# Performance work log

Measured on AMD Instinct MI355X. Metric: run time of the kernel, lower is better.

The kernel has to match this reference:

```python
import jax, jax.numpy as jnp
import numpy as np

H = 16          # num attention heads (== num kv heads here)
D = 128         # head_dim
HID = 2048      # hidden_size = H * D
THETA = 10000.0
SCALE = 1.0 / (D ** 0.5)
EPS = 1e-8


def rotate_half(x):
    x1, x2 = x[..., : D // 2], x[..., D // 2 :]
    return jnp.concatenate((-x2, x1), axis=-1)


def rope_tables(seq_len):
    inv_freq = 1.0 / (THETA ** (jnp.arange(0, D, 2, dtype=jnp.float32) / D))
    freqs = jnp.outer(jnp.arange(seq_len, dtype=jnp.float32), inv_freq)  # [S, D/2]
    emb = jnp.concatenate((freqs, freqs), axis=-1)                        # [S, D]
    return jnp.cos(emb), jnp.sin(emb)


def setup_inputs() -> dict:
    key = jax.random.key(0)
    ks = jax.random.split(key, 10)
    B, S = 1, 2048
    hidden_states = jax.random.normal(ks[0], (B, S, HID), jnp.float32) * 0.02
    position_ids = jnp.tile(jnp.arange(S, dtype=jnp.int32)[None, :], (B, 1))
    # additive causal mask, shape (B, 1, S, S) as asserted in the torch forward
    causal = jnp.tril(jnp.ones((S, S), dtype=bool))
    attention_mask = jnp.where(causal, 0.0, -1e9).astype(jnp.float32)[None, None]
    attention_mask = jnp.tile(attention_mask, (B, 1, 1, 1))
    Wq = jax.random.normal(ks[1], (HID, HID), jnp.float32) * 0.02
    bq = jax.random.normal(ks[2], (HID,), jnp.float32) * 0.02
    Wk = jax.random.normal(ks[3], (HID, HID), jnp.float32) * 0.02
    bk = jax.random.normal(ks[4], (HID,), jnp.float32) * 0.02
    Wo = jax.random.normal(ks[5], (HID, HID), jnp.float32) * 0.02
    beta = jax.random.normal(ks[6], (1,), jnp.float32)
    M = jax.random.normal(ks[7], (H, D, D), jnp.float32) * 0.02
    z = jax.random.uniform(ks[8], (H, D), jnp.float32) * 100.0 + 1.0  # positive accumulator
    return {
        "hidden_states": hidden_states,
        "attention_mask": attention_mask,
        "position_ids": position_ids,
        "Wq": Wq, "bq": bq, "Wk": Wk, "bk": bk, "Wo": Wo,
        "beta": beta, "M": M, "z": z,
    }


def reference(hidden_states, attention_mask, position_ids, Wq, bq, Wk, bk, Wo, beta, M, z):
    B, S, _ = hidden_states.shape
    # projections (NOTE: source uses q_proj for value_states too -- reproduced faithfully)
    q = (hidden_states @ Wq + bq).reshape(B, S, H, D).transpose(0, 2, 1, 3)  # [B,H,S,D]
    k = (hidden_states @ Wk + bk).reshape(B, S, H, D).transpose(0, 2, 1, 3)
    v = q  # value_states = q_proj(hidden_states), no RoPE applied to values

    cos, sin = rope_tables(S)
    cos = cos[position_ids][:, None]  # [B,1,S,D]
    sin = sin[position_ids][:, None]
    qr = q * cos + rotate_half(q) * sin
    kr = k * cos + rotate_half(k) * sin

    # --- compressive memory retrieval (with pre-update M, z) ---
    sq = jax.nn.elu(qr) + 1.0                                  # [B,H,S,D]
    mem_num = jnp.einsum('bhsd,hde->bhse', sq, M)              # [B,H,S,D]
    mem_den = jnp.einsum('bhsd,hd->bhs', sq, z)[..., None] + EPS
    memory_output = mem_num / mem_den

    # --- memory update: outer-product accumulation ---
    sk = jax.nn.elu(kr) + 1.0
    M_new = M + jnp.einsum('bhsd,bhse->hde', sk, v)
    z_new = z + sk.sum(axis=(0, 2))

    # --- local attention (SDPA with additive mask, dropout 0) ---
    scores = jnp.einsum('bhsd,bhtd->bhst', qr, kr) * SCALE + attention_mask
    probs = jax.nn.softmax(scores, axis=-1)
    attn_output = jnp.einsum('bhst,bhtd->bhsd', probs, v)

    # --- long-term memory injection: sigmoid-gated blend ---
    g = jax.nn.sigmoid(beta)[0]
    combined = g * memory_output + (1.0 - g) * attn_output     # [B,H,S,D]
    combined = combined.transpose(0, 2, 1, 3).reshape(B, S, HID)
    final_output = combined @ Wo
    return (final_output, M_new, z_new)
```

## Files before the change

### kernel.cpp

```cpp
#include <hip/hip_runtime.h>
#include <hip/hip_bf16.h>


#define S_LEN 2048
#define HID 2048
#define NH 16
#define HD 128
#define SCALE_QK 0.088388347648318447f

typedef __attribute__((ext_vector_type(8))) short bf16x8;
typedef __attribute__((ext_vector_type(4))) float f32x4;

__device__ __forceinline__ short f2bf(float f) {
  __hip_bfloat16 h = __float2bfloat16(f);
  return __builtin_bit_cast(short, h);
}
__device__ __forceinline__ float bf2f(short s) {
  unsigned int u = ((unsigned int)(unsigned short)s) << 16;
  return __builtin_bit_cast(float, u);
}
__device__ __forceinline__ void gload16(const void* g, void* l) {
  __builtin_amdgcn_global_load_lds(
      (const __attribute__((address_space(1))) void*)g,
      (__attribute__((address_space(3))) void*)l, 16, 0, 0);
}

__global__ __launch_bounds__(256) void f32_to_bf16_kernel(
    const float* __restrict__ in, short* __restrict__ out) {
  size_t i = (size_t)(blockIdx.x * 256 + threadIdx.x) * 8;
  float4 a = *reinterpret_cast<const float4*>(in + i);
  float4 b = *reinterpret_cast<const float4*>(in + i + 4);
  alignas(16) short t[8] = {f2bf(a.x), f2bf(a.y), f2bf(a.z), f2bf(a.w),
                            f2bf(b.x), f2bf(b.y), f2bf(b.z), f2bf(b.w)};
  *reinterpret_cast<int4*>(out + i) = *reinterpret_cast<int4*>(t);
}

__global__ __launch_bounds__(256) void transpose_f2b_kernel(
    const float* __restrict__ in, short* __restrict__ out, int R, int C) {
  __shared__ float t[32][33];
  size_t bo = (size_t)blockIdx.z * R * C;
  int r0 = blockIdx.y * 32, c0 = blockIdx.x * 32;
  int tx = threadIdx.x & 31, ty = threadIdx.x >> 5;
#pragma unroll
  for (int i = 0; i < 4; ++i)
    t[ty + i * 8][tx] = in[bo + (size_t)(r0 + ty + i * 8) * C + c0 + tx];
  __syncthreads();
#pragma unroll
  for (int i = 0; i < 4; ++i)
    out[bo + (size_t)(c0 + ty + i * 8) * R + r0 + tx] = f2bf(t[tx][ty + i * 8]);
}

__global__ __launch_bounds__(256) void transpose_b2b_kernel(
    const short* __restrict__ in, short* __restrict__ out, int R, int C) {
  __shared__ short t[32][33];
  int r0 = blockIdx.y * 32, c0 = blockIdx.x * 32;
  int tx = threadIdx.x & 31, ty = threadIdx.x >> 5;
#pragma unroll
  for (int i = 0; i < 4; ++i)
    t[ty + i * 8][tx] = in[(size_t)(r0 + ty + i * 8) * C + c0 + tx];
  __syncthreads();
#pragma unroll
  for (int i = 0; i < 4; ++i)
    out[(size_t)(c0 + ty + i * 8) * R + r0 + tx] = t[tx][ty + i * 8];
}

__global__ __launch_bounds__(256) void tables_kernel(
    const int* __restrict__ pos_ids, float* __restrict__ cost,
    float* __restrict__ sint) {
  int idx = blockIdx.x * 256 + threadIdx.x;
  int s = idx >> 6, j = idx & 63;
  float pos = (float)pos_ids[s];
  float inv = powf(10000.0f, -((float)j) / 64.0f);
  float a = pos * inv;
  cost[idx] = cosf(a);
  sint[idx] = sinf(a);
}

__global__ __launch_bounds__(256) void gemm_qk_rope_kernel(
    const short* __restrict__ A, const short* __restrict__ BT,
    const float* __restrict__ bq, const float* __restrict__ bk,
    const float* __restrict__ cost, const float* __restrict__ sint,
    short* __restrict__ qr, short* __restrict__ kr, short* __restrict__ sq,
    short* __restrict__ sk, short* __restrict__ v) {
  __shared__ __align__(16) char smem[67584];
  const int K = 2048;
  const int tid = threadIdx.x;
  const int wave = tid >> 6, lane = tid & 63;
  const int g = lane >> 4, l15 = lane & 15;
  const int wm = (wave >> 1) * 64, wn = (wave & 1) * 64;
  const int row0 = blockIdx.x * 128;
  const int colg0 = blockIdx.y * 128;

  const int ld_r = wave * 32 + (lane >> 3);
  const int ld_c = (lane & 7) * 8;
  const short* Ag = A + (size_t)(row0 + ld_r) * K + ld_c;
  const short* Bg = BT + (size_t)(colg0 + ld_r) * K + ld_c;

#define GSTAGE(BUF, KT)                                                       \
  {                                                                           \
    _Pragma("unroll") for (int i = 0; i < 4; ++i) {                           \
      gload16(Ag + (size_t)(KT) * 64 + (size_t)i * 8 * 2048,                  \
              smem + (BUF) * 32768 + wave * 4096 + i * 1024);                 \
      gload16(Bg + (size_t)(KT) * 64 + (size_t)i * 8 * 2048,                  \
              smem + (BUF) * 32768 + 16384 + wave * 4096 + i * 1024);         \
    }                                                                         \
  }

  f32x4 acc[4][4] = {};
  GSTAGE(0, 0);
  __syncthreads();
  for (int kt = 0; kt < 32; ++kt) {
    const int cur = kt & 1;
    if (kt + 1 < 32) GSTAGE(cur ^ 1, kt + 1);
#pragma unroll
    for (int ks = 0; ks < 2; ++ks) {
      bf16x8 a[4], b[4];
#pragma unroll
      for (int m = 0; m < 4; ++m)
        a[m] = *reinterpret_cast<bf16x8*>(smem + cur * 32768 +
                                          (wm + m * 16 + l15) * 128 +
                                          (ks * 32 + g * 8) * 2);
#pragma unroll
      for (int n = 0; n < 4; ++n)
        b[n] = *reinterpret_cast<bf16x8*>(smem + cur * 32768 + 16384 +
                                          (wn + n * 16 + l15) * 128 +
                                          (ks * 32 + g * 8) * 2);
#pragma unroll
      for (int m = 0; m < 4; ++m)
#pragma unroll
        for (int n = 0; n < 4; ++n)
          acc[m][n] = __builtin_amdgcn_mfma_f32_16x16x32_bf16(a[m], b[n],
                                                              acc[m][n], 0, 0, 0);
    }
    __syncthreads();
  }
#undef GSTAGE

  const bool qpath = (colg0 < 2048);
  const int col0 = qpath ? colg0 : colg0 - 2048;
  const float* bias = qpath ? bq : bk;
  float* qb = reinterpret_cast<float*>(smem);
#pragma unroll
  for (int m = 0; m < 4; ++m)
#pragma unroll
    for (int n = 0; n < 4; ++n) {
      int rl = wm + m * 16 + g * 4;
      int cl = wn + n * 16 + l15;
      float bv = bias[col0 + cl];
#pragma unroll
      for (int r = 0; r < 4; ++r) qb[(rl + r) * 132 + cl] = acc[m][n][r] + bv;
    }
  __syncthreads();

  const int rl = tid >> 1;
  const int c0 = (tid & 1) * 64;
  const int rowg = row0 + rl;
  const float sgn = (c0 == 0) ? -1.0f : 1.0f;
  const size_t obase = (size_t)rowg * HID + col0 + c0;
#pragma unroll
  for (int j0 = 0; j0 < 64; j0 += 8) {
    alignas(16) short o1[8], o2[8], o3[8];
#pragma unroll
    for (int jj = 0; jj < 8; ++jj) {
      int j = j0 + jj;
      float self = qb[rl * 132 + c0 + j];
      float part = qb[rl * 132 + (c0 ^ 64) + j];
      float cs = cost[rowg * 64 + j];
      float sn = sint[rowg * 64 + j];
      float rv = self * cs + sgn * part * sn;
      o1[jj] = f2bf(rv);
      o2[jj] = f2bf(rv > 0.0f ? rv + 1.0f : __expf(rv));
      o3[jj] = f2bf(self);
    }
    if (qpath) {
      *reinterpret_cast<int4*>(qr + obase + j0) = *reinterpret_cast<int4*>(o1);
      *reinterpret_cast<int4*>(sq + obase + j0) = *reinterpret_cast<int4*>(o2);
      *reinterpret_cast<int4*>(v + obase + j0) = *reinterpret_cast<int4*>(o3);
    } else {
      *reinterpret_cast<int4*>(kr + obase + j0) = *reinterpret_cast<int4*>(o1);
      *reinterpret_cast<int4*>(sk + obase + j0) = *reinterpret_cast<int4*>(o2);
    }
  }
}

__global__ __launch_bounds__(256) void gemm_wo_kernel(
    const short* __restrict__ A, const short* __restrict__ BT,
    float* __restrict__ C) {
  __shared__ __align__(16) char smem[65536];
  const int K = 2048;
  const int tid = threadIdx.x;
  const int wave = tid >> 6, lane = tid & 63;
  const int g = lane >> 4, l15 = lane & 15;
  const int wm = (wave >> 1) * 64, wn = (wave & 1) * 64;
  const int row0 = blockIdx.x * 128;
  const int col0 = blockIdx.y * 128;

  const int ld_r = wave * 32 + (lane >> 3);
  const int ld_c = (lane & 7) * 8;
  const short* Ag = A + (size_t)(row0 + ld_r) * K + ld_c;
  const short* Bg = BT + (size_t)(col0 + ld_r) * K + ld_c;

#define GSTAGE(BUF, KT)                                                       \
  {                                                                           \
    _Pragma("unroll") for (int i = 0; i < 4; ++i) {                           \
      gload16(Ag + (size_t)(KT) * 64 + (size_t)i * 8 * 2048,                  \
              smem + (BUF) * 32768 + wave * 4096 + i * 1024);                 \
      gload16(Bg + (size_t)(KT) * 64 + (size_t)i * 8 * 2048,                  \
              smem + (BUF) * 32768 + 16384 + wave * 4096 + i * 1024);         \
    }                                                                         \
  }

  f32x4 acc[4][4] = {};
  GSTAGE(0, 0);
  __syncthreads();
  for (int kt = 0; kt < 32; ++kt) {
    const int cur = kt & 1;
    if (kt + 1 < 32) GSTAGE(cur ^ 1, kt + 1);
#pragma unroll
    for (int ks = 0; ks < 2; ++ks) {
      bf16x8 a[4], b[4];
#pragma unroll
      for (int m = 0; m < 4; ++m)
        a[m] = *reinterpret_cast<bf16x8*>(smem + cur * 32768 +
                                          (wm + m * 16 + l15) * 128 +
                                          (ks * 32 + g * 8) * 2);
#pragma unroll
      for (int n = 0; n < 4; ++n)
        b[n] = *reinterpret_cast<bf16x8*>(smem + cur * 32768 + 16384 +
                                          (wn + n * 16 + l15) * 128 +
                                          (ks * 32 + g * 8) * 2);
#pragma unroll
      for (int m = 0; m < 4; ++m)
#pragma unroll
        for (int n = 0; n < 4; ++n)
          acc[m][n] = __builtin_amdgcn_mfma_f32_16x16x32_bf16(a[m], b[n],
                                                              acc[m][n], 0, 0, 0);
    }
    __syncthreads();
  }
#undef GSTAGE

#pragma unroll
  for (int m = 0; m < 4; ++m)
#pragma unroll
    for (int n = 0; n < 4; ++n) {
      int row = row0 + wm + m * 16 + g * 4;
      int col = col0 + wn + n * 16 + l15;
#pragma unroll
      for (int r = 0; r < 4; ++r)
        C[(size_t)(row + r) * 2048 + col] = acc[m][n][r];
    }
}

__global__ __launch_bounds__(256) void attn_kernel(
    const short* __restrict__ qr, const short* __restrict__ kr,
    const short* __restrict__ vT, const short* __restrict__ sq,
    const short* __restrict__ MT, const float* __restrict__ z,
    const float* __restrict__ beta, short* __restrict__ comb) {
  __shared__ short k_s[2][64 * 128];
  __shared__ short v_s[2][128 * 64];
  __shared__ short p_s[4][16 * 64];
  const int tid = threadIdx.x;
  const int wave = tid >> 6, lane = tid & 63;
  const int g = lane >> 4, l15 = lane & 15;
  const int bid = blockIdx.x;
  const int h = bid & 15;
  const int u = bid >> 4;
  const int qt = (u < 16) ? (2 * u) : (31 - 2 * (u - 16));
  const int q0 = qt * 64;
  const int ntiles = qt + 1;

  const int krow_b = wave * 16 + (lane >> 4);
  const int vrow_b = wave * 32 + (lane >> 3);
#define STAGE_TILE(B, T0)                                                     \
  {                                                                           \
    _Pragma("unroll") for (int i = 0; i < 4; ++i) {                           \
      int rk = krow_b + i * 4;                                                \
      int ck = (lane & 15) ^ (rk & 7);                                        \
      gload16(kr + (size_t)((T0) + rk) * HID + h * HD + ck * 8,               \
              &k_s[B][0] + wave * 2048 + i * 512);                            \
      int rv = vrow_b + i * 8;                                                \
      int cv = (lane & 7) ^ (rv & 7);                                         \
      gload16(vT + (size_t)(h * HD + rv) * S_LEN + (T0) + cv * 8,             \
              &v_s[B][0] + wave * 2048 + i * 512);                            \
    }                                                                         \
  }

  bf16x8 qf[4];
#pragma unroll
  for (int ks = 0; ks < 4; ++ks) {
    int row = q0 + wave * 16 + l15;
    qf[ks] = *reinterpret_cast<const bf16x8*>(qr + (size_t)row * HID + h * HD +
                                              ks * 32 + g * 8);
  }

  STAGE_TILE(0, 0);
  __syncthreads();

  f32x4 o[8] = {};
  float m_run[4], l_run[4];
#pragma unroll
  for (int r = 0; r < 4; ++r) {
    m_run[r] = -3.0e38f;
    l_run[r] = 0.0f;
  }

  for (int kt = 0; kt < ntiles; ++kt) {
    const int cur = kt & 1;
    if (kt + 1 < ntiles) STAGE_TILE(cur ^ 1, (kt + 1) * 64);

    f32x4 sfr[4] = {};
    __builtin_amdgcn_s_setprio(1);
#pragma unroll
    for (int n = 0; n < 4; ++n) {
#pragma unroll
      for (int ks = 0; ks < 4; ++ks) {
        int rr = n * 16 + l15;
        int off = (rr * 256 + (ks * 32 + g * 8) * 2) ^ ((rr & 7) << 4);
        bf16x8 b =
            *reinterpret_cast<bf16x8*>(reinterpret_cast<char*>(k_s[cur]) + off);
        sfr[n] = __builtin_amdgcn_mfma_f32_16x16x32_bf16(qf[ks], b, sfr[n], 0,
                                                         0, 0);
      }
    }
    __builtin_amdgcn_s_setprio(0);

    const bool diag = (kt == qt);
#pragma unroll
    for (int r = 0; r < 4; ++r) {
      const int srow = q0 + wave * 16 + g * 4 + r;
      float mx = m_run[r];
#pragma unroll
      for (int n = 0; n < 4; ++n) {
        float val = sfr[n][r] * SCALE_QK;
        if (diag) {
          int t = kt * 64 + n * 16 + l15;
          val = (t <= srow) ? val : -3.0e38f;
        }
        sfr[n][r] = val;
        mx = fmaxf(mx, val);
      }
      mx = fmaxf(mx, __shfl_xor(mx, 1));
      mx = fmaxf(mx, __shfl_xor(mx, 2));
      mx = fmaxf(mx, __shfl_xor(mx, 4));
      mx = fmaxf(mx, __shfl_xor(mx, 8));
      float sum = 0.0f;
#pragma unroll
      for (int n = 0; n < 4; ++n) {
        float p = __expf(sfr[n][r] - mx);
        sfr[n][r] = p;
        sum += p;
      }
      sum += __shfl_xor(sum, 1);
      sum += __shfl_xor(sum, 2);
      sum += __shfl_xor(sum, 4);
      sum += __shfl_xor(sum, 8);
      float f = __expf(m_run[r] - mx);
      l_run[r] = l_run[r] * f + sum;
      m_run[r] = mx;
#pragma unroll
      for (int n = 0; n < 8; ++n) o[n][r] *= f;
    }

    char* pw = reinterpret_cast<char*>(p_s[wave]);
#pragma unroll
    for (int n = 0; n < 4; ++n)
#pragma unroll
      for (int r = 0; r < 4; ++r) {
        int rl = g * 4 + r;
        int off = (rl * 128 + (n * 16 + l15) * 2) ^ ((rl & 7) << 4);
        *reinterpret_cast<short*>(pw + off) = f2bf(sfr[n][r]);
      }

    __builtin_amdgcn_s_setprio(1);
#pragma unroll
    for (int ks = 0; ks < 2; ++ks) {
      int offp = (l15 * 128 + (ks * 32 + g * 8) * 2) ^ ((l15 & 7) << 4);
      bf16x8 pa = *reinterpret_cast<bf16x8*>(pw + offp);
#pragma unroll
      for (int n = 0; n < 8; ++n) {
        int rr = n * 16 + l15;
        int off = (rr * 128 + (ks * 32 + g * 8) * 2) ^ ((rr & 7) << 4);
        bf16x8 vb =
            *reinterpret_cast<bf16x8*>(reinterpret_cast<char*>(v_s[cur]) + off);
        o[n] = __builtin_amdgcn_mfma_f32_16x16x32_bf16(pa, vb, o[n], 0, 0, 0);
      }
    }
    __builtin_amdgcn_s_setprio(0);

    __syncthreads();
  }
#undef STAGE_TILE

  short* mt_s = &k_s[0][0];
#pragma unroll
  for (int i = 0; i < 8; ++i) {
    int c = tid + 256 * i;
    int r = c >> 4, kc = c & 15;
    int4 d = *reinterpret_cast<const int4*>(MT + (size_t)h * 16384 + r * 128 +
                                            kc * 8);
    *reinterpret_cast<int4*>(reinterpret_cast<char*>(mt_s) +
                             ((r * 256 + kc * 16) ^ ((r & 7) << 4))) = d;
  }
  __syncthreads();

  bf16x8 af[4];
#pragma unroll
  for (int ks = 0; ks < 4; ++ks) {
    int row = q0 + wave * 16 + l15;
    af[ks] = *reinterpret_cast<const bf16x8*>(sq + (size_t)row * HID + h * HD +
                                              ks * 32 + g * 8);
  }
  f32x4 acc2[8] = {};
#pragma unroll
  for (int ks = 0; ks < 4; ++ks) {
#pragma unroll
    for (int n = 0; n < 8; ++n) {
      int rr = n * 16 + l15;
      int off = (rr * 256 + (ks * 32 + g * 8) * 2) ^ ((rr & 7) << 4);
      bf16x8 b =
          *reinterpret_cast<bf16x8*>(reinterpret_cast<char*>(mt_s) + off);
      acc2[n] = __builtin_amdgcn_mfma_f32_16x16x32_bf16(af[ks], b, acc2[n], 0,
                                                        0, 0);
    }
  }

  float den[4];
#pragma unroll
  for (int r = 0; r < 4; ++r) {
    int row = q0 + wave * 16 + g * 4 + r;
    bf16x8 sv = *reinterpret_cast<const bf16x8*>(sq + (size_t)row * HID +
                                                 h * HD + l15 * 8);
    float part = 0.0f;
#pragma unroll
    for (int j = 0; j < 8; ++j) part += bf2f(sv[j]) * z[h * HD + l15 * 8 + j];
    part += __shfl_xor(part, 1);
    part += __shfl_xor(part, 2);
    part += __shfl_xor(part, 4);
    part += __shfl_xor(part, 8);
    den[r] = part + 1e-8f;
  }

  float gv = 1.0f / (1.0f + __expf(-beta[0]));
#pragma unroll
  for (int n = 0; n < 8; ++n)
#pragma unroll
    for (int r = 0; r < 4; ++r) {
      int row = q0 + wave * 16 + g * 4 + r;
      int col = n * 16 + l15;
      float mem = acc2[n][r] / den[r];
      float at = o[n][r] / l_run[r];
      comb[(size_t)row * HID + h * HD + col] = f2bf(gv * mem + (1.0f - gv) * at);
    }
}

__global__ __launch_bounds__(256) void mnew_part_kernel(
    const short* __restrict__ skT, const short* __restrict__ vT,
    float* __restrict__ part) {
  const int sp = blockIdx.x;
  const int h = blockIdx.y;
  const int tid = threadIdx.x;
  const int wave = tid >> 6, lane = tid & 63;
  const int g = lane >> 4, l15 = lane & 15;
  f32x4 acc[2][8] = {};
  for (int ks = sp * 8; ks < sp * 8 + 8; ++ks) {
    bf16x8 a[2];
#pragma unroll
    for (int m = 0; m < 2; ++m) {
      int dd = wave * 32 + m * 16 + l15;
      a[m] = *reinterpret_cast<const bf16x8*>(skT + (size_t)(h * HD + dd) * S_LEN +
                                              ks * 32 + g * 8);
    }
#pragma unroll
    for (int n = 0; n < 8; ++n) {
      int e = n * 16 + l15;
      bf16x8 b = *reinterpret_cast<const bf16x8*>(
          vT + (size_t)(h * HD + e) * S_LEN + ks * 32 + g * 8);
#pragma unroll
      for (int m = 0; m < 2; ++m)
        acc[m][n] =
            __builtin_amdgcn_mfma_f32_16x16x32_bf16(a[m], b, acc[m][n], 0, 0, 0);
    }
  }
#pragma unroll
  for (int m = 0; m < 2; ++m)
#pragma unroll
    for (int n = 0; n < 8; ++n)
#pragma unroll
      for (int r = 0; r < 4; ++r) {
        int dd = wave * 32 + m * 16 + g * 4 + r;
        int e = n * 16 + l15;
        part[(size_t)(sp * 16 + h) * 16384 + (size_t)dd * 128 + e] =
            acc[m][n][r];
      }
}

__global__ __launch_bounds__(256) void mnew_reduce_kernel(
    const float* __restrict__ part, const float* __restrict__ Mold,
    float* __restrict__ Mout) {
  int idx = blockIdx.x * 256 + threadIdx.x;
  int j4 = idx * 4;
  int h = j4 >> 14;
  int rem = j4 & 16383;
  float4 a = *reinterpret_cast<const float4*>(Mold + j4);
#pragma unroll
  for (int s = 0; s < 8; ++s) {
    float4 p = *reinterpret_cast<const float4*>(
        part + ((size_t)(s * 16 + h) << 14) + rem);
    a.x += p.x;
    a.y += p.y;
    a.z += p.z;
    a.w += p.w;
  }
  *reinterpret_cast<float4*>(Mout + j4) = a;
}

__global__ __launch_bounds__(256) void znew_kernel(const short* __restrict__ skT,
                                                   const float* __restrict__ z,
                                                   float* __restrict__ out) {
  int row = blockIdx.x;
  int tid = threadIdx.x;
  bf16x8 vv = *reinterpret_cast<const bf16x8*>(skT + (size_t)row * S_LEN + tid * 8);
  float s = 0.0f;
#pragma unroll
  for (int j = 0; j < 8; ++j) s += bf2f(vv[j]);
#pragma unroll
  for (int off = 1; off < 64; off <<= 1) s += __shfl_xor(s, off);
  __shared__ float wsum[4];
  if ((tid & 63) == 0) wsum[tid >> 6] = s;
  __syncthreads();
  if (tid == 0) out[row] = z[row] + wsum[0] + wsum[1] + wsum[2] + wsum[3];
}

extern "C" void kernel_launch(void* const* d_in, const int* in_sizes, int n_in,
                              void* d_out, int out_size, void* d_ws,
                              size_t ws_size, hipStream_t stream) {
  const float* hs = (const float*)d_in[0];
  const int* pos = (const int*)d_in[2];
  const float* Wq = (const float*)d_in[3];
  const float* bq = (const float*)d_in[4];
  const float* Wk = (const float*)d_in[5];
  const float* bk = (const float*)d_in[6];
  const float* Wo = (const float*)d_in[7];
  const float* beta = (const float*)d_in[8];
  const float* Mm = (const float*)d_in[9];
  const float* z = (const float*)d_in[10];
  float* out = (float*)d_out;

  char* ws = (char*)d_ws;
  const size_t MB = 1u << 20;
  short* hs_b = (short*)(ws + 0);
  short* WqkT = (short*)(ws + 8 * MB);
  short* WoT = (short*)(ws + 24 * MB);
  short* qr = (short*)(ws + 32 * MB);
  short* kr = (short*)(ws + 40 * MB);
  short* sq = (short*)(ws + 48 * MB);
  short* sk = (short*)(ws + 56 * MB);
  short* v = (short*)(ws + 64 * MB);
  short* comb = (short*)(ws + 72 * MB);
  short* MT = (short*)(ws + 80 * MB);
  float* cost = (float*)(ws + 80 * MB + 512 * 1024);
  float* sint = (float*)(ws + 81 * MB);
  short* skT = WqkT;
  short* vT = WqkT + 4 * 1024 * 1024;
  float* mpart = (float*)hs_b;

  f32_to_bf16_kernel<<<2048, 256, 0, stream>>>(hs, hs_b);
  transpose_f2b_kernel<<<dim3(64, 64, 1), 256, 0, stream>>>(Wq, WqkT, 2048, 2048);
  transpose_f2b_kernel<<<dim3(64, 64, 1), 256, 0, stream>>>(
      Wk, WqkT + 4 * 1024 * 1024, 2048, 2048);
  transpose_f2b_kernel<<<dim3(64, 64, 1), 256, 0, stream>>>(Wo, WoT, 2048, 2048);
  transpose_f2b_kernel<<<dim3(4, 4, 16), 256, 0, stream>>>(Mm, MT, 128, 128);
  tables_kernel<<<512, 256, 0, stream>>>(pos, cost, sint);

  gemm_qk_rope_kernel<<<dim3(16, 32), 256, 0, stream>>>(
      hs_b, WqkT, bq, bk, cost, sint, qr, kr, sq, sk, v);
  transpose_b2b_kernel<<<dim3(64, 64, 1), 256, 0, stream>>>(v, vT, 2048, 2048);
  transpose_b2b_kernel<<<dim3(64, 64, 1), 256, 0, stream>>>(sk, skT, 2048, 2048);

  attn_kernel<<<512, 256, 0, stream>>>(qr, kr, vT, sq, MT, z, beta, comb);
  gemm_wo_kernel<<<dim3(16, 16), 256, 0, stream>>>(comb, WoT, out);
  mnew_part_kernel<<<dim3(8, 16), 256, 0, stream>>>(skT, vT, mpart);
  mnew_reduce_kernel<<<256, 256, 0, stream>>>(mpart, Mm, out + 4194304);
  znew_kernel<<<2048, 256, 0, stream>>>(skT, z, out + 4194304 + 16 * 128 * 128);
}
```

Before: 356.8 us.

## Split causal attention KV range across blocks, fuse transposes into QK epilogue

The QK projection epilogue now writes skT and vT directly in transposed layout, which removes the two standalone bf16 transpose kernels. Attention now uses 512-thread blocks covering 128 query rows, with the KV range split into two halves that run as separate blocks. Each half writes partial outputs plus its running max and sum, and a new combine kernel merges them and applies the memory retrieval and gating. This is meant to balance causal work across blocks and cut transpose traffic, at the cost of extra partial-output round trips through memory and one more launch. Online softmax also skips rescaling unless the running max grows by more than 8.

New measurement: 368.8 us. +3.4%, slower.

```diff
diff --git a/kernel.cpp b/kernel.cpp
--- a/kernel.cpp
+++ b/kernel.cpp
@@ -48,20 +48,6 @@
 #pragma unroll
   for (int i = 0; i < 4; ++i)
     out[bo + (size_t)(c0 + ty + i * 8) * R + r0 + tx] = f2bf(t[tx][ty + i * 8]);
-}
-
-__global__ __launch_bounds__(256) void transpose_b2b_kernel(
-    const short* __restrict__ in, short* __restrict__ out, int R, int C) {
-  __shared__ short t[32][33];
-  int r0 = blockIdx.y * 32, c0 = blockIdx.x * 32;
-  int tx = threadIdx.x & 31, ty = threadIdx.x >> 5;
-#pragma unroll
-  for (int i = 0; i < 4; ++i)
-    t[ty + i * 8][tx] = in[(size_t)(r0 + ty + i * 8) * C + c0 + tx];
-  __syncthreads();
-#pragma unroll
-  for (int i = 0; i < 4; ++i)
-    out[(size_t)(c0 + ty + i * 8) * R + r0 + tx] = t[tx][ty + i * 8];
 }
 
 __global__ __launch_bounds__(256) void tables_kernel(
@@ -81,9 +67,8 @@
     const float* __restrict__ bq, const float* __restrict__ bk,
     const float* __restrict__ cost, const float* __restrict__ sint,
     short* __restrict__ qr, short* __restrict__ kr, short* __restrict__ sq,
-    short* __restrict__ sk, short* __restrict__ v) {
+    short* __restrict__ skT, short* __restrict__ vT) {
   __shared__ __align__(16) char smem[67584];
-  const int K = 2048;
   const int tid = threadIdx.x;
   const int wave = tid >> 6, lane = tid & 63;
   const int g = lane >> 4, l15 = lane & 15;
@@ -93,8 +78,8 @@
 
   const int ld_r = wave * 32 + (lane >> 3);
   const int ld_c = (lane & 7) * 8;
-  const short* Ag = A + (size_t)(row0 + ld_r) * K + ld_c;
-  const short* Bg = BT + (size_t)(colg0 + ld_r) * K + ld_c;
+  const short* Ag = A + (size_t)(row0 + ld_r) * 2048 + ld_c;
+  const short* Bg = BT + (size_t)(colg0 + ld_r) * 2048 + ld_c;
 
 #define GSTAGE(BUF, KT)                                                       \
   {                                                                           \
@@ -138,6 +123,7 @@
 
   const bool qpath = (colg0 < 2048);
   const int col0 = qpath ? colg0 : colg0 - 2048;
+  const int hh = col0 >> 7;
   const float* bias = qpath ? bq : bk;
   float* qb = reinterpret_cast<float*>(smem);
 #pragma unroll
@@ -152,33 +138,61 @@
     }
   __syncthreads();
 
-  const int rl = tid >> 1;
-  const int c0 = (tid & 1) * 64;
-  const int rowg = row0 + rl;
-  const float sgn = (c0 == 0) ? -1.0f : 1.0f;
-  const size_t obase = (size_t)rowg * HID + col0 + c0;
-#pragma unroll
-  for (int j0 = 0; j0 < 64; j0 += 8) {
-    alignas(16) short o1[8], o2[8], o3[8];
-#pragma unroll
-    for (int jj = 0; jj < 8; ++jj) {
-      int j = j0 + jj;
-      float self = qb[rl * 132 + c0 + j];
-      float part = qb[rl * 132 + (c0 ^ 64) + j];
-      float cs = cost[rowg * 64 + j];
-      float sn = sint[rowg * 64 + j];
-      float rv = self * cs + sgn * part * sn;
-      o1[jj] = f2bf(rv);
-      o2[jj] = f2bf(rv > 0.0f ? rv + 1.0f : __expf(rv));
-      o3[jj] = f2bf(self);
-    }
-    if (qpath) {
-      *reinterpret_cast<int4*>(qr + obase + j0) = *reinterpret_cast<int4*>(o1);
-      *reinterpret_cast<int4*>(sq + obase + j0) = *reinterpret_cast<int4*>(o2);
-      *reinterpret_cast<int4*>(v + obase + j0) = *reinterpret_cast<int4*>(o3);
-    } else {
-      *reinterpret_cast<int4*>(kr + obase + j0) = *reinterpret_cast<int4*>(o1);
-      *reinterpret_cast<int4*>(sk + obase + j0) = *reinterpret_cast<int4*>(o2);
+  {
+    const int rl = tid >> 1;
+    const int c0 = (tid & 1) * 64;
+    const int rowg = row0 + rl;
+    const float sgn = (c0 == 0) ? -1.0f : 1.0f;
+    const size_t obase = (size_t)rowg * HID + col0 + c0;
+#pragma unroll
+    for (int j0 = 0; j0 < 64; j0 += 8) {
+      alignas(16) short o1[8], o2[8];
+#pragma unroll
+      for (int jj = 0; jj < 8; ++jj) {
+        int j = j0 + jj;
+        float self = qb[rl * 132 + c0 + j];
+        float part = qb[rl * 132 + (c0 ^ 64) + j];
+        float cs = cost[rowg * 64 + j];
+        float sn = sint[rowg * 64 + j];
+        float rv = self * cs + sgn * part * sn;
+        o1[jj] = f2bf(rv);
+        o2[jj] = f2bf(rv > 0.0f ? rv + 1.0f : __expf(rv));
+      }
+      if (qpath) {
+        *reinterpret_cast<int4*>(qr + obase + j0) = *reinterpret_cast<int4*>(o1);
+        *reinterpret_cast<int4*>(sq + obase + j0) = *reinterpret_cast<int4*>(o2);
+      } else {
+        *reinterpret_cast<int4*>(kr + obase + j0) = *reinterpret_cast<int4*>(o1);
+      }
+    }
+  }
+
+  {
+    const int d = tid & 127;
+    const int sc = tid >> 7;
+    const int dp = d ^ 64;
+    const float sgn2 = (d < 64) ? -1.0f : 1.0f;
+    short* dstb = (qpath ? vT : skT) + (size_t)(hh * HD + d) * S_LEN + row0 +
+                  sc * 64;
+#pragma unroll
+    for (int j0 = 0; j0 < 64; j0 += 8) {
+      alignas(16) short ot[8];
+#pragma unroll
+      for (int jj = 0; jj < 8; ++jj) {
+        int s = sc * 64 + j0 + jj;
+        float self = qb[s * 132 + d];
+        if (qpath) {
+          ot[jj] = f2bf(self);
+        } else {
+          float part = qb[s * 132 + dp];
+          int rowg = row0 + s;
+          float cs = cost[rowg * 64 + (d & 63)];
+          float sn = sint[rowg * 64 + (d & 63)];
+          float rv = self * cs + sgn2 * part * sn;
+          ot[jj] = f2bf(rv > 0.0f ? rv + 1.0f : __expf(rv));
+        }
+      }
+      *reinterpret_cast<int4*>(dstb + j0) = *reinterpret_cast<int4*>(ot);
     }
   }
 }
@@ -187,7 +201,6 @@
     const short* __restrict__ A, const short* __restrict__ BT,
     float* __restrict__ C) {
   __shared__ __align__(16) char smem[65536];
-  const int K = 2048;
   const int tid = threadIdx.x;
   const int wave = tid >> 6, lane = tid & 63;
   const int g = lane >> 4, l15 = lane & 15;
@@ -197,8 +210,8 @@
 
   const int ld_r = wave * 32 + (lane >> 3);
   const int ld_c = (lane & 7) * 8;
-  const short* Ag = A + (size_t)(row0 + ld_r) * K + ld_c;
-  const short* Bg = BT + (size_t)(col0 + ld_r) * K + ld_c;
+  const short* Ag = A + (size_t)(row0 + ld_r) * 2048 + ld_c;
+  const short* Bg = BT + (size_t)(col0 + ld_r) * 2048 + ld_c;
 
 #define GSTAGE(BUF, KT)                                                       \
   {                                                                           \
@@ -252,37 +265,38 @@
     }
 }
 
-__global__ __launch_bounds__(256) void attn_kernel(
+__global__ __launch_bounds__(512, 4) void attn_kernel(
     const short* __restrict__ qr, const short* __restrict__ kr,
-    const short* __restrict__ vT, const short* __restrict__ sq,
-    const short* __restrict__ MT, const float* __restrict__ z,
-    const float* __restrict__ beta, short* __restrict__ comb) {
+    const short* __restrict__ vT, short* __restrict__ opart,
+    float* __restrict__ ml) {
   __shared__ short k_s[2][64 * 128];
   __shared__ short v_s[2][128 * 64];
-  __shared__ short p_s[4][16 * 64];
+  __shared__ short p_s[8][16 * 64];
   const int tid = threadIdx.x;
   const int wave = tid >> 6, lane = tid & 63;
   const int g = lane >> 4, l15 = lane & 15;
   const int bid = blockIdx.x;
   const int h = bid & 15;
-  const int u = bid >> 4;
-  const int qt = (u < 16) ? (2 * u) : (31 - 2 * (u - 16));
-  const int q0 = qt * 64;
-  const int ntiles = qt + 1;
-
-  const int krow_b = wave * 16 + (lane >> 4);
-  const int vrow_b = wave * 32 + (lane >> 3);
+  const int w = bid >> 4;
+  const int half = (w < 16) ? 0 : 1;
+  const int qt = (w < 16) ? w : 31 - w;
+  const int q0 = qt * 128;
+  const int jstart = half ? (qt + 1) : 0;
+  const int jend = half ? (2 * qt + 2) : (qt + 1);
+
+  const int krow_b = wave * 8 + (lane >> 4);
+  const int vrow_b = wave * 16 + (lane >> 3);
 #define STAGE_TILE(B, T0)                                                     \
   {                                                                           \
-    _Pragma("unroll") for (int i = 0; i < 4; ++i) {                           \
+    _Pragma("unroll") for (int i = 0; i < 2; ++i) {                           \
       int rk = krow_b + i * 4;                                                \
       int ck = (lane & 15) ^ (rk & 7);                                        \
       gload16(kr + (size_t)((T0) + rk) * HID + h * HD + ck * 8,               \
-              &k_s[B][0] + wave * 2048 + i * 512);                            \
+              &k_s[B][0] + wave * 1024 + i * 512);                            \
       int rv = vrow_b + i * 8;                                                \
       int cv = (lane & 7) ^ (rv & 7);                                         \
       gload16(vT + (size_t)(h * HD + rv) * S_LEN + (T0) + cv * 8,             \
-              &v_s[B][0] + wave * 2048 + i * 512);                            \
+              &v_s[B][0] + wave * 1024 + i * 512);                            \
     }                                                                         \
   }
 
@@ -294,7 +308,7 @@
                                               ks * 32 + g * 8);
   }
 
-  STAGE_TILE(0, 0);
+  STAGE_TILE(0, jstart * 64);
   __syncthreads();
 
   f32x4 o[8] = {};
@@ -305,9 +319,9 @@
     l_run[r] = 0.0f;
   }
 
-  for (int kt = 0; kt < ntiles; ++kt) {
-    const int cur = kt & 1;
-    if (kt + 1 < ntiles) STAGE_TILE(cur ^ 1, (kt + 1) * 64);
+  for (int j = jstart; j < jend; ++j) {
+    const int cur = (j - jstart) & 1;
+    if (j + 1 < jend) STAGE_TILE(cur ^ 1, (j + 1) * 64);
 
     f32x4 sfr[4] = {};
     __builtin_amdgcn_s_setprio(1);
@@ -325,29 +339,36 @@
     }
     __builtin_amdgcn_s_setprio(0);
 
-    const bool diag = (kt == qt);
+    const bool diag = (j >= 2 * qt);
 #pragma unroll
     for (int r = 0; r < 4; ++r) {
       const int srow = q0 + wave * 16 + g * 4 + r;
-      float mx = m_run[r];
+      float pmax = -3.0e38f;
 #pragma unroll
       for (int n = 0; n < 4; ++n) {
         float val = sfr[n][r] * SCALE_QK;
         if (diag) {
-          int t = kt * 64 + n * 16 + l15;
+          int t = j * 64 + n * 16 + l15;
           val = (t <= srow) ? val : -3.0e38f;
         }
         sfr[n][r] = val;
-        mx = fmaxf(mx, val);
-      }
-      mx = fmaxf(mx, __shfl_xor(mx, 1));
-      mx = fmaxf(mx, __shfl_xor(mx, 2));
-      mx = fmaxf(mx, __shfl_xor(mx, 4));
-      mx = fmaxf(mx, __shfl_xor(mx, 8));
+        pmax = fmaxf(pmax, val);
+      }
+      pmax = fmaxf(pmax, __shfl_xor(pmax, 1));
+      pmax = fmaxf(pmax, __shfl_xor(pmax, 2));
+      pmax = fmaxf(pmax, __shfl_xor(pmax, 4));
+      pmax = fmaxf(pmax, __shfl_xor(pmax, 8));
+      if (pmax > m_run[r] + 8.0f) {
+        float f = __expf(m_run[r] - pmax);
+        l_run[r] *= f;
+#pragma unroll
+        for (int n = 0; n < 8; ++n) o[n][r] *= f;
+        m_run[r] = pmax;
+      }
       float sum = 0.0f;
 #pragma unroll
       for (int n = 0; n < 4; ++n) {
-        float p = __expf(sfr[n][r] - mx);
+        float p = __expf(sfr[n][r] - m_run[r]);
         sfr[n][r] = p;
         sum += p;
       }
@@ -355,11 +376,7 @@
       sum += __shfl_xor(sum, 2);
       sum += __shfl_xor(sum, 4);
       sum += __shfl_xor(sum, 8);
-      float f = __expf(m_run[r] - mx);
-      l_run[r] = l_run[r] * f + sum;
-      m_run[r] = mx;
-#pragma unroll
-      for (int n = 0; n < 8; ++n) o[n][r] *= f;
+      l_run[r] += sum;
     }
 
     char* pw = reinterpret_cast<char*>(p_s[wave]);
@@ -392,7 +409,34 @@
   }
 #undef STAGE_TILE
 
-  short* mt_s = &k_s[0][0];
+  const size_t ob = (size_t)half * 4194304;
+#pragma unroll
+  for (int r = 0; r < 4; ++r) {
+    int row = q0 + wave * 16 + g * 4 + r;
+#pragma unroll
+    for (int n = 0; n < 8; ++n) {
+      int col = n * 16 + l15;
+      opart[ob + (size_t)row * HID + h * HD + col] = f2bf(o[n][r]);
+    }
+    if (l15 == 0) {
+      size_t mli = ((size_t)(half * 16 + h) * 2048 + row) * 2;
+      ml[mli] = m_run[r];
+      ml[mli + 1] = l_run[r];
+    }
+  }
+}
+
+__global__ __launch_bounds__(256) void combine_kernel(
+    const short* __restrict__ opart, const float* __restrict__ ml,
+    const short* __restrict__ sq, const short* __restrict__ MT,
+    const float* __restrict__ z, const float* __restrict__ beta,
+    short* __restrict__ comb) {
+  __shared__ short mt_s[128 * 128];
+  const int tid = threadIdx.x;
+  const int wave = tid >> 6, lane = tid & 63;
+  const int g = lane >> 4, l15 = lane & 15;
+  const int h = blockIdx.y;
+  const int s0 = blockIdx.x * 128;
 #pragma unroll
   for (int i = 0; i < 8; ++i) {
     int c = tid + 256 * i;
@@ -404,53 +448,68 @@
   }
   __syncthreads();
 
-  bf16x8 af[4];
+  f32x4 acc[2][8] = {};
 #pragma unroll
   for (int ks = 0; ks < 4; ++ks) {
-    int row = q0 + wave * 16 + l15;
-    af[ks] = *reinterpret_cast<const bf16x8*>(sq + (size_t)row * HID + h * HD +
+    bf16x8 a[2];
+#pragma unroll
+    for (int m = 0; m < 2; ++m) {
+      int row = s0 + wave * 32 + m * 16 + l15;
+      a[m] = *reinterpret_cast<const bf16x8*>(sq + (size_t)row * HID + h * HD +
                                               ks * 32 + g * 8);
-  }
-  f32x4 acc2[8] = {};
-#pragma unroll
-  for (int ks = 0; ks < 4; ++ks) {
+    }
 #pragma unroll
     for (int n = 0; n < 8; ++n) {
       int rr = n * 16 + l15;
       int off = (rr * 256 + (ks * 32 + g * 8) * 2) ^ ((rr & 7) << 4);
-      bf16x8 b =
-          *reinterpret_cast<bf16x8*>(reinterpret_cast<char*>(mt_s) + off);
-      acc2[n] = __builtin_amdgcn_mfma_f32_16x16x32_bf16(af[ks], b, acc2[n], 0,
-                                                        0, 0);
-    }
-  }
-
-  float den[4];
-#pragma unroll
-  for (int r = 0; r < 4; ++r) {
-    int row = q0 + wave * 16 + g * 4 + r;
-    bf16x8 sv = *reinterpret_cast<const bf16x8*>(sq + (size_t)row * HID +
-                                                 h * HD + l15 * 8);
-    float part = 0.0f;
-#pragma unroll
-    for (int j = 0; j < 8; ++j) part += bf2f(sv[j]) * z[h * HD + l15 * 8 + j];
-    part += __shfl_xor(part, 1);
-    part += __shfl_xor(part, 2);
-    part += __shfl_xor(part, 4);
-    part += __shfl_xor(part, 8);
-    den[r] = part + 1e-8f;
-  }
-
+      bf16x8 b = *reinterpret_cast<bf16x8*>(reinterpret_cast<char*>(mt_s) + off);
+#pragma unroll
+      for (int m = 0; m < 2; ++m)
+        acc[m][n] =
+            __builtin_amdgcn_mfma_f32_16x16x32_bf16(a[m], b, acc[m][n], 0, 0, 0);
+    }
+  }
+
+  float den[2][4];
+#pragma unroll
+  for (int m = 0; m < 2; ++m)
+#pragma unroll
+    for (int r = 0; r < 4; ++r) {
+      int row = s0 + wave * 32 + m * 16 + g * 4 + r;
+      bf16x8 sv = *reinterpret_cast<const bf16x8*>(sq + (size_t)row * HID +
+                                                   h * HD + l15 * 8);
+      float part = 0.0f;
+#pragma unroll
+      for (int j = 0; j < 8; ++j) part += bf2f(sv[j]) * z[h * HD + l15 * 8 + j];
+      part += __shfl_xor(part, 1);
+      part += __shfl_xor(part, 2);
+      part += __shfl_xor(part, 4);
+      part += __shfl_xor(part, 8);
+      den[m][r] = part + 1e-8f;
+    }
   float gv = 1.0f / (1.0f + __expf(-beta[0]));
 #pragma unroll
-  for (int n = 0; n < 8; ++n)
+  for (int m = 0; m < 2; ++m)
 #pragma unroll
     for (int r = 0; r < 4; ++r) {
-      int row = q0 + wave * 16 + g * 4 + r;
-      int col = n * 16 + l15;
-      float mem = acc2[n][r] / den[r];
-      float at = o[n][r] / l_run[r];
-      comb[(size_t)row * HID + h * HD + col] = f2bf(gv * mem + (1.0f - gv) * at);
+      int row = s0 + wave * 32 + m * 16 + g * 4 + r;
+      float m0 = ml[((size_t)h * 2048 + row) * 2];
+      float l0 = ml[((size_t)h * 2048 + row) * 2 + 1];
+      float m1 = ml[((size_t)(16 + h) * 2048 + row) * 2];
+      float l1 = ml[((size_t)(16 + h) * 2048 + row) * 2 + 1];
+      float mm = fmaxf(m0, m1);
+      float e0 = __expf(m0 - mm), e1 = __expf(m1 - mm);
+      float inv = 1.0f / (l0 * e0 + l1 * e1);
+#pragma unroll
+      for (int n = 0; n < 8; ++n) {
+        int col = n * 16 + l15;
+        float a0 = bf2f(opart[(size_t)row * HID + h * HD + col]);
+        float a1 = bf2f(opart[4194304 + (size_t)row * HID + h * HD + col]);
+        float at = (a0 * e0 + a1 * e1) * inv;
+        float mem = acc[m][n][r] / den[m][r];
+        comb[(size_t)row * HID + h * HD + col] =
+            f2bf(gv * mem + (1.0f - gv) * at);
+      }
     }
 }
 
@@ -555,15 +614,15 @@
   short* qr = (short*)(ws + 32 * MB);
   short* kr = (short*)(ws + 40 * MB);
   short* sq = (short*)(ws + 48 * MB);
-  short* sk = (short*)(ws + 56 * MB);
-  short* v = (short*)(ws + 64 * MB);
+  short* skT = (short*)(ws + 56 * MB);
+  short* vT = (short*)(ws + 64 * MB);
   short* comb = (short*)(ws + 72 * MB);
   short* MT = (short*)(ws + 80 * MB);
   float* cost = (float*)(ws + 80 * MB + 512 * 1024);
   float* sint = (float*)(ws + 81 * MB);
-  short* skT = WqkT;
-  short* vT = WqkT + 4 * 1024 * 1024;
-  float* mpart = (float*)hs_b;
+  short* opart = hs_b;
+  float* ml = (float*)(ws + 16 * MB);
+  float* mpart = (float*)(ws + 0);
 
   f32_to_bf16_kernel<<<2048, 256, 0, stream>>>(hs, hs_b);
   transpose_f2b_kernel<<<dim3(64, 64, 1), 256, 0, stream>>>(Wq, WqkT, 2048, 2048);
@@ -574,11 +633,11 @@
   tables_kernel<<<512, 256, 0, stream>>>(pos, cost, sint);
 
   gemm_qk_rope_kernel<<<dim3(16, 32), 256, 0, stream>>>(
-      hs_b, WqkT, bq, bk, cost, sint, qr, kr, sq, sk, v);
-  transpose_b2b_kernel<<<dim3(64, 64, 1), 256, 0, stream>>>(v, vT, 2048, 2048);
-  transpose_b2b_kernel<<<dim3(64, 64, 1), 256, 0, stream>>>(sk, skT, 2048, 2048);
-
-  attn_kernel<<<512, 256, 0, stream>>>(qr, kr, vT, sq, MT, z, beta, comb);
+      hs_b, WqkT, bq, bk, cost, sint, qr, kr, sq, skT, vT);
+
+  attn_kernel<<<512, 512, 0, stream>>>(qr, kr, vT, opart, ml);
+  combine_kernel<<<dim3(16, 16), 256, 0, stream>>>(opart, ml, sq, MT, z, beta,
+                                                   comb);
   gemm_wo_kernel<<<dim3(16, 16), 256, 0, stream>>>(comb, WoT, out);
   mnew_part_kernel<<<dim3(8, 16), 256, 0, stream>>>(skT, vT, mpart);
   mnew_reduce_kernel<<<256, 256, 0, stream>>>(mpart, Mm, out + 4194304);
```
